# Kernel optimization log

Measured on AMD Instinct MI355X. Metric: run time of the kernel, lower is better.

The kernel has to match this reference:

```python
import jax, jax.numpy as jnp
import numpy as np
from jax import lax

INPUT_DIM = 32
OUTPUT_DIM = 32
INPUT_ATOMS = 8
OUTPUT_ATOMS = 8
KERNEL = 5
NUM_ROUTING = 3
B = 8
H = W = 32


def setup_inputs() -> dict:
    key = jax.random.key(0)
    k1, k2, k3 = jax.random.split(key, 3)
    x = jax.random.normal(k1, (B * INPUT_DIM, INPUT_ATOMS, H, W), jnp.float32)
    conv_w = jax.random.normal(k2, (KERNEL, KERNEL, INPUT_ATOMS, OUTPUT_DIM * OUTPUT_ATOMS), jnp.float32) * 0.05
    conv_b = jnp.zeros((OUTPUT_DIM * OUTPUT_ATOMS,), jnp.float32)
    biases = jax.random.normal(k3, (OUTPUT_DIM, OUTPUT_ATOMS, 1, 1), jnp.float32) * 0.1
    return {"x": x, "conv_w": conv_w, "conv_b": conv_b, "biases": biases}


def _squash(s):
    # squash over the atom axis (axis=2), matching tf _squash
    norm = jnp.sqrt(jnp.sum(s * s, axis=2, keepdims=True))
    norm_sq = norm * norm
    return (s / norm) * (norm_sq / (1.0 + norm_sq))


def reference(x, conv_w, conv_b, biases):
    # x: [B*input_dim, input_atoms, H, W]; conv: channels_first, SAME padding
    out = lax.conv_general_dilated(
        x, conv_w, window_strides=(1, 1), padding='SAME',
        dimension_numbers=('NCHW', 'HWIO', 'NCHW')) + conv_b[None, :, None, None]
    h, w = out.shape[2], out.shape[3]
    b = x.shape[0] // INPUT_DIM
    # votes: [b, i, o, a, h, w]
    votes = out.reshape(b, INPUT_DIM, OUTPUT_DIM, OUTPUT_ATOMS, h, w)
    logits = jnp.zeros((b, INPUT_DIM, OUTPUT_DIM, h, w), votes.dtype)
    leak = jnp.zeros((b, INPUT_DIM, 1, h, w), votes.dtype)
    act = None
    for it in range(NUM_ROUTING):
        # leaky softmax over output_dim axis (extra zero logit, then dropped)
        route = jax.nn.softmax(jnp.concatenate([leak, logits], axis=2), axis=2)[:, :, 1:]
        preact = jnp.einsum('bioahw,biohw->boahw', votes, route) + biases  # [b,o,a,h,w]
        act = _squash(preact)
        if it < NUM_ROUTING - 1:
            logits = logits + jnp.einsum('bioahw,boahw->biohw', votes, act)
    # [b, o, h, w, a] -> [b, o*h*w, 8]
    act = jnp.transpose(act, (0, 1, 3, 4, 2))
    return act.reshape(b, -1, 8)
```

## Files before the change

### kernel.cpp

```cpp
#include <hip/hip_runtime.h>
#include <math.h>


using short8 = __attribute__((ext_vector_type(8))) short;
using f32x4  = __attribute__((ext_vector_type(4))) float;

__device__ __forceinline__ unsigned short f2bf(float f) {
    unsigned u = __float_as_uint(f);
    return (unsigned short)((u + 0x7fffu + ((u >> 16) & 1u)) >> 16);
}

template<int CTRL>
__device__ __forceinline__ float dpp_movf(float x) {
    return __int_as_float(__builtin_amdgcn_update_dpp(
        0, __float_as_int(x), CTRL, 0xF, 0xF, true));
}
__device__ __forceinline__ float swz_xor4(float x) {
    return __int_as_float(__builtin_amdgcn_ds_swizzle(__float_as_int(x), 0x101F));
}
__device__ __forceinline__ float sum8(float x) {
    x += dpp_movf<0xB1>(x);
    x += dpp_movf<0x4E>(x);
    x += dpp_movf<0x141>(x);
    return x;
}
__device__ __forceinline__ float max8(float x) {
    x = fmaxf(x, dpp_movf<0xB1>(x));
    x = fmaxf(x, dpp_movf<0x4E>(x));
    x = fmaxf(x, dpp_movf<0x141>(x));
    return x;
}
__device__ __forceinline__ float reduce_xpose8(float p[8]) {
    p[0] += dpp_movf<0xB1>(p[1]);
    p[2] += dpp_movf<0xB1>(p[3]);
    p[4] += dpp_movf<0xB1>(p[5]);
    p[6] += dpp_movf<0xB1>(p[7]);
    p[0] += dpp_movf<0x4E>(p[2]);
    p[4] += dpp_movf<0x4E>(p[6]);
    p[0] += swz_xor4(p[4]);
    return p[0];
}

__global__ __launch_bounds__(256)
void prep_w(const float* __restrict__ cw, unsigned short* __restrict__ wp) {
    const int idx = blockIdx.x * 256 + threadIdx.x;
    const int j  = idx & 7;
    const int oa = (idx >> 3) & 255;
    const int g  = (idx >> 11) & 3;
    const int s  = idx >> 13;
    const int k  = s * 32 + g * 8 + j;
    wp[idx] = (k < 200) ? f2bf(cw[k * 256 + oa]) : (unsigned short)0;
}

__global__ __launch_bounds__(256)
void prep_x(const float* __restrict__ x, unsigned short* __restrict__ xt) {
    __shared__ unsigned short tile[32 * 256];
    const int t = threadIdx.x;
    const int b = blockIdx.x >> 5, y = blockIdx.x & 31;
    const float* src = x + (((size_t)((b << 8) + t)) << 10) + (y << 5);
    #pragma unroll
    for (int c = 0; c < 8; ++c) {
        float4 v = *(const float4*)(src + c * 4);
        tile[(c * 4 + 0) * 256 + t] = f2bf(v.x);
        tile[(c * 4 + 1) * 256 + t] = f2bf(v.y);
        tile[(c * 4 + 2) * 256 + t] = f2bf(v.z);
        tile[(c * 4 + 3) * 256 + t] = f2bf(v.w);
    }
    __syncthreads();
    unsigned short* dst = xt + ((size_t)blockIdx.x << 13);
    #pragma unroll
    for (int c = 0; c < 4; ++c) {
        const int chunk = t + c * 256;
        *(short8*)(dst + chunk * 8) = *(const short8*)(&tile[chunk * 8]);
    }
}

__global__ __launch_bounds__(512, 4)
void capsule_mfma2(const unsigned short* __restrict__ xt,
                   const unsigned short* __restrict__ wp,
                   const float* __restrict__ conv_b,
                   const float* __restrict__ biases,
                   float* __restrict__ out)
{
    __shared__ __align__(16) char lds[40960];

    const int t   = threadIdx.x;
    const int blk = blockIdx.x;
    const int b   = blk >> 9;
    const int rem = blk & 511;
    const int h   = rem >> 4;
    const int w0  = (rem & 15) << 1;

    for (int u = t; u < 960; u += 512) {
        const int i = u & 31, pos = u >> 5;
        const int ky = pos / 6, xl = pos - ky * 6;
        const int y = h + ky - 2, xx = w0 + xl - 2;
        short8 vv = {0, 0, 0, 0, 0, 0, 0, 0};
        if ((unsigned)y < 32u && (unsigned)xx < 32u)
            vv = *(const short8*)(xt + (((size_t)(((b << 5) + y) << 5) + xx) << 8) + i * 8);
        *(short8*)(lds + i * 496 + pos * 16) = vv;
    }

    const int l  = t & 63, wv = t >> 6;
    const int lm = l & 15, lg = l >> 4;
    const int o_l = l >> 3, ig = l & 7;
    const int o  = ((wv & 3) << 3) + o_l;
    const int q  = wv >> 2;

    const float cb_own   = conv_b[t & 255];
    const float bias_own = biases[t & 255];

    f32x4 acc[4][2];
    #pragma unroll
    for (int mt = 0; mt < 4; ++mt)
        #pragma unroll
        for (int ti = 0; ti < 2; ++ti)
            acc[mt][ti] = (f32x4){0.f, 0.f, 0.f, 0.f};

    __syncthreads();

    const unsigned short* wbase = wp + lg * 2048 + ((((wv & 3) << 6) + lm) << 3);

    #pragma unroll
    for (int s = 0; s < 7; ++s) {
        short8 a[4];
        #pragma unroll
        for (int mt = 0; mt < 4; ++mt)
            a[mt] = *(const short8*)(wbase + s * 8192 + mt * 128);
        const int kt = s * 4 + lg;
        int pos = 0;
        if (kt <= 24) { const int ky = kt / 5; pos = ky * 6 + (kt - ky * 5); }
        const char* bb = lds + (pos + q) * 16;
        const short8 b0 = *(const short8*)(bb + lm * 496);
        const short8 b1 = *(const short8*)(bb + (16 + lm) * 496);
        #pragma unroll
        for (int mt = 0; mt < 4; ++mt) {
            acc[mt][0] = __builtin_amdgcn_mfma_f32_16x16x32_bf16(a[mt], b0, acc[mt][0], 0, 0, 0);
            acc[mt][1] = __builtin_amdgcn_mfma_f32_16x16x32_bf16(a[mt], b1, acc[mt][1], 0, 0, 0);
        }
    }

    __syncthreads();

    float v[4][8];
    char* vtrb = lds + wv * 5120;
    const int wbyte = lg * 320 + lm * 4;
    const int rbase = o_l * 640 + (ig & 3) * 16;
    #pragma unroll
    for (int ro = 0; ro < 2; ++ro) {
        #pragma unroll
        for (int mt = 0; mt < 4; ++mt)
            #pragma unroll
            for (int r = 0; r < 4; ++r)
                *(float*)(vtrb + wbyte + mt * 1280 + r * 80) = acc[mt][ro][r];
        if ((ig >> 2) == ro) {
            #pragma unroll
            for (int j = 0; j < 8; ++j) {
                const int a = ig ^ j;
                const f32x4 r4 = *(const f32x4*)(vtrb + rbase + a * 80);
                v[0][j] = r4[0]; v[1][j] = r4[1]; v[2][j] = r4[2]; v[3][j] = r4[3];
            }
        }
    }
    __syncthreads();

    float* logits_q = (float*)(lds + q * 4608);
    float* route_q  = (float*)(lds + 9216 + q * 4608);
    const int rw_byte = ig * 576 + o * 4;
    const int sm_byte = o * 144 + (ig << 4);

    float lacc[4] = {0.f, 0.f, 0.f, 0.f};
    float actv = 0.f;

    #pragma unroll
    for (int it = 0; it < 3; ++it) {
        float pre;
        if (it == 0) {
            float p[8];
            #pragma unroll
            for (int j = 0; j < 8; ++j)
                p[j] = (v[0][j] + v[1][j]) + (v[2][j] + v[3][j]);
            const float R = reduce_xpose8(p);
            pre = fmaf(fmaf(cb_own, 32.f, R), 1.f / 33.f, bias_own);
        } else {
            float r4[4];
            #pragma unroll
            for (int di = 0; di < 4; ++di)
                r4[di] = *(const float*)((char*)route_q + rw_byte + di * 144);
            float p[8];
            #pragma unroll
            for (int j = 0; j < 8; ++j) {
                float s = v[0][j] * r4[0];
                s = fmaf(v[1][j], r4[1], s);
                s = fmaf(v[2][j], r4[2], s);
                s = fmaf(v[3][j], r4[3], s);
                p[j] = s;
            }
            const float S_o = sum8((r4[0] + r4[1]) + (r4[2] + r4[3]));
            const float P = reduce_xpose8(p);
            pre = fmaf(cb_own, S_o, P) + bias_own;
        }

        const float ns = sum8(pre * pre);
        actv = pre * ns * __builtin_amdgcn_rsqf(ns) * __builtin_amdgcn_rcpf(1.f + ns);

        if (it < 2) {
            float ag[8];
            ag[0] = actv;
            ag[4] = swz_xor4(ag[0]);
            ag[2] = dpp_movf<0x4E>(ag[0]);
            ag[6] = dpp_movf<0x4E>(ag[4]);
            ag[1] = dpp_movf<0xB1>(ag[0]);
            ag[3] = dpp_movf<0xB1>(ag[2]);
            ag[5] = dpp_movf<0xB1>(ag[4]);
            ag[7] = dpp_movf<0xB1>(ag[6]);
            const float cbact = sum8(cb_own * actv);

            #pragma unroll
            for (int di = 0; di < 4; ++di) {
                float d = cbact;
                #pragma unroll
                for (int j = 0; j < 8; ++j)
                    d = fmaf(v[di][j], ag[j], d);
                lacc[di] += d;
                *(float*)((char*)logits_q + rw_byte + di * 144) = lacc[di];
            }
            __syncthreads();

            f32x4 e = *(const f32x4*)((char*)logits_q + sm_byte);
            float mx = fmaxf(fmaxf(e[0], e[1]), fmaxf(e[2], e[3]));
            mx = max8(fmaxf(mx, 0.f));
            e[0] = __expf(e[0] - mx); e[1] = __expf(e[1] - mx);
            e[2] = __expf(e[2] - mx); e[3] = __expf(e[3] - mx);
            const float ssum = sum8((e[0] + e[1]) + (e[2] + e[3])) + __expf(-mx);
            const float inv = __builtin_amdgcn_rcpf(ssum);
            e[0] *= inv; e[1] *= inv; e[2] *= inv; e[3] *= inv;
            *(f32x4*)((char*)route_q + sm_byte) = e;
            __syncthreads();
        }
    }

    const int pix = (h << 5) + w0 + q;
    out[(((size_t)(((b << 5) + o) << 10) + pix) << 3) + ig] = actv;
}

extern "C" void kernel_launch(void* const* d_in, const int* in_sizes, int n_in,
                              void* d_out, int out_size, void* d_ws, size_t ws_size,
                              hipStream_t stream) {
    const float* x      = (const float*)d_in[0];
    const float* conv_w = (const float*)d_in[1];
    const float* conv_b = (const float*)d_in[2];
    const float* biases = (const float*)d_in[3];
    unsigned short* wp = (unsigned short*)d_ws;
    unsigned short* xt = (unsigned short*)((char*)d_ws + 131072);
    prep_w<<<dim3(224), dim3(256), 0, stream>>>(conv_w, wp);
    prep_x<<<dim3(256), dim3(256), 0, stream>>>(x, xt);
    capsule_mfma2<<<dim3(4096), dim3(512), 0, stream>>>(xt, wp, conv_b, biases, (float*)d_out);
}
```

Measured before the change: 69.39 us.

## Swizzle LDS layouts, prefetch first weights, drop barriers around vote transpose

```diff
diff --git a/kernel.cpp b/kernel.cpp
--- a/kernel.cpp
+++ b/kernel.cpp
@@ -82,7 +82,7 @@
                    const float* __restrict__ biases,
                    float* __restrict__ out)
 {
-    __shared__ __align__(16) char lds[40960];
+    __shared__ __align__(16) char lds[38912];
 
     const int t   = threadIdx.x;
     const int blk = blockIdx.x;
@@ -98,7 +98,7 @@
         short8 vv = {0, 0, 0, 0, 0, 0, 0, 0};
         if ((unsigned)y < 32u && (unsigned)xx < 32u)
             vv = *(const short8*)(xt + (((size_t)(((b << 5) + y) << 5) + xx) << 8) + i * 8);
-        *(short8*)(lds + i * 496 + pos * 16) = vv;
+        *(short8*)(lds + i * 512 + ((pos ^ (i & 15)) << 4)) = vv;
     }
 
     const int l  = t & 63, wv = t >> 6;
@@ -110,6 +110,12 @@
     const float cb_own   = conv_b[t & 255];
     const float bias_own = biases[t & 255];
 
+    const unsigned short* wbase = wp + lg * 2048 + ((((wv & 3) << 6) + lm) << 3);
+    short8 a0[4];
+    #pragma unroll
+    for (int mt = 0; mt < 4; ++mt)
+        a0[mt] = *(const short8*)(wbase + mt * 128);
+
     f32x4 acc[4][2];
     #pragma unroll
     for (int mt = 0; mt < 4; ++mt)
@@ -119,50 +125,53 @@
 
     __syncthreads();
 
-    const unsigned short* wbase = wp + lg * 2048 + ((((wv & 3) << 6) + lm) << 3);
-
     #pragma unroll
     for (int s = 0; s < 7; ++s) {
         short8 a[4];
         #pragma unroll
         for (int mt = 0; mt < 4; ++mt)
-            a[mt] = *(const short8*)(wbase + s * 8192 + mt * 128);
+            a[mt] = (s == 0) ? a0[mt]
+                             : *(const short8*)(wbase + s * 8192 + mt * 128);
         const int kt = s * 4 + lg;
         int pos = 0;
         if (kt <= 24) { const int ky = kt / 5; pos = ky * 6 + (kt - ky * 5); }
-        const char* bb = lds + (pos + q) * 16;
-        const short8 b0 = *(const short8*)(bb + lm * 496);
-        const short8 b1 = *(const short8*)(bb + (16 + lm) * 496);
+        const int pr = pos + q;
+        const short8 b0 = *(const short8*)(lds + lm * 512 + ((pr ^ lm) << 4));
+        const short8 b1 = *(const short8*)(lds + (16 + lm) * 512 + ((pr ^ lm) << 4));
+        __builtin_amdgcn_s_setprio(1);
         #pragma unroll
         for (int mt = 0; mt < 4; ++mt) {
             acc[mt][0] = __builtin_amdgcn_mfma_f32_16x16x32_bf16(a[mt], b0, acc[mt][0], 0, 0, 0);
             acc[mt][1] = __builtin_amdgcn_mfma_f32_16x16x32_bf16(a[mt], b1, acc[mt][1], 0, 0, 0);
         }
-    }
-
-    __syncthreads();
+        __builtin_amdgcn_s_setprio(0);
+    }
 
     float v[4][8];
-    char* vtrb = lds + wv * 5120;
-    const int wbyte = lg * 320 + lm * 4;
-    const int rbase = o_l * 640 + (ig & 3) * 16;
-    #pragma unroll
-    for (int ro = 0; ro < 2; ++ro) {
-        #pragma unroll
-        for (int mt = 0; mt < 4; ++mt)
-            #pragma unroll
-            for (int r = 0; r < 4; ++r)
-                *(float*)(vtrb + wbyte + mt * 1280 + r * 80) = acc[mt][ro][r];
-        if ((ig >> 2) == ro) {
-            #pragma unroll
-            for (int j = 0; j < 8; ++j) {
-                const int a = ig ^ j;
-                const f32x4 r4 = *(const f32x4*)(vtrb + rbase + a * 80);
-                v[0][j] = r4[0]; v[1][j] = r4[1]; v[2][j] = r4[2]; v[3][j] = r4[3];
+    char* vtrb = lds + 18432 + wv * 2560;
+    #pragma unroll
+    for (int mh = 0; mh < 2; ++mh)
+        #pragma unroll
+        for (int ro = 0; ro < 2; ++ro) {
+            #pragma unroll
+            for (int m2 = 0; m2 < 2; ++m2)
+                #pragma unroll
+                for (int r = 0; r < 4; ++r) {
+                    const int row = (m2 << 4) + (lg << 2) + r;
+                    *(float*)(vtrb + row * 80 +
+                              ((((lm >> 2) + (row >> 3)) & 3) << 4) + ((lm & 3) << 2)) =
+                        acc[mh * 2 + m2][ro][r];
+                }
+            if ((ig >> 2) == ro && (o_l >> 2) == mh) {
+                const int cph = (((ig & 3) + (o_l & 3)) & 3) << 4;
+                #pragma unroll
+                for (int j = 0; j < 8; ++j) {
+                    const int row = ((o_l & 3) << 3) + (ig ^ j);
+                    const f32x4 r4 = *(const f32x4*)(vtrb + row * 80 + cph);
+                    v[0][j] = r4[0]; v[1][j] = r4[1]; v[2][j] = r4[2]; v[3][j] = r4[3];
+                }
             }
         }
-    }
-    __syncthreads();
 
     float* logits_q = (float*)(lds + q * 4608);
     float* route_q  = (float*)(lds + 9216 + q * 4608);
@@ -223,8 +232,13 @@
                 for (int j = 0; j < 8; ++j)
                     d = fmaf(v[di][j], ag[j], d);
                 lacc[di] += d;
+            }
+
+            if (it == 0) __syncthreads();
+
+            #pragma unroll
+            for (int di = 0; di < 4; ++di)
                 *(float*)((char*)logits_q + rw_byte + di * 144) = lacc[di];
-            }
             __syncthreads();
 
             f32x4 e = *(const f32x4*)((char*)logits_q + sm_byte);
```

Result: no change. 68.23 us (-1.7%).
